# Optimization experiments

Hardware: AMD Instinct MI355X
Metric: run time of the kernel (lower is better)

Reference implementation:

```python
import jax, jax.numpy as jnp
import numpy as np

C = jnp.complex64

def _ry_mat(t):
    c = jnp.cos(t / 2).astype(C)
    s = jnp.sin(t / 2).astype(C)
    return jnp.stack([jnp.stack([c, -s], -1), jnp.stack([s, c], -1)], -2)

def _rx_mat(t):
    c = jnp.cos(t / 2).astype(C)
    s = (-1j) * jnp.sin(t / 2).astype(C)
    return jnp.stack([jnp.stack([c, s], -1), jnp.stack([s, c], -1)], -2)

def _rz_mat(t):
    em = jnp.exp(-1j * (t / 2).astype(C))
    ep = jnp.exp(1j * (t / 2).astype(C))
    z = jnp.zeros_like(em)
    return jnp.stack([jnp.stack([em, z], -1), jnp.stack([z, ep], -1)], -2)

def _apply_1q(psi, gate, w):
    # psi: [bsz, 2^n]; gate: [2,2] (shared) or [bsz,2,2] (per-sample)
    bsz = psi.shape[0]
    s = psi.reshape(bsz, 1 << w, 2, -1)  # wire w isolated on axis 2
    if gate.ndim == 2:
        out = jnp.einsum('ij,bljr->blir', gate, s)
    else:
        out = jnp.einsum('bij,bljr->blir', gate, s)
    return out.reshape(bsz, -1)

def _apply_cnot(psi, c, t):
    bsz = psi.shape[0]
    a, b = min(c, t), max(c, t)
    s = psi.reshape(bsz, 1 << a, 2, 1 << (b - a - 1), 2, -1)
    if c < t:
        # control on axis 2, target on axis 4; after slicing ctrl=1, target -> axis 3
        s = s.at[:, :, 1].set(jnp.flip(s[:, :, 1], axis=3))
    else:
        # control on axis 4, target on axis 2
        s = s.at[:, :, :, :, 1].set(jnp.flip(s[:, :, :, :, 1], axis=2))
    return s.reshape(bsz, -1)

def setup_inputs() -> dict:
    key = jax.random.key(0)
    k1, k2 = jax.random.split(key)
    bsz, n_wires, n_qlayers = 1024, 14, 4
    x_raw = jax.random.normal(k1, (bsz, n_wires), dtype=jnp.float32)
    angles = jax.random.normal(k2, (n_qlayers, n_wires, 3), dtype=jnp.float32) * 0.1
    return {"x_raw": x_raw, "angles": angles}

def reference(x_raw, angles):
    L, n, _ = angles.shape
    bsz = x_raw.shape[0]
    x_enc = jnp.tanh(x_raw[:, :n]) * jnp.pi  # [bsz, n]
    # |0...0> statevector, wire 0 is the most significant bit
    psi = jnp.zeros((bsz, 1 << n), dtype=C).at[:, 0].set(1.0)
    # RY encoding (per-sample angles)
    for w in range(n):
        psi = _apply_1q(psi, _ry_mat(x_enc[:, w]), w)
    # variational layers
    for k in range(L):
        for w in range(n):
            psi = _apply_1q(psi, _rx_mat(angles[k, w, 0]), w)
            psi = _apply_1q(psi, _ry_mat(angles[k, w, 1]), w)
            psi = _apply_1q(psi, _rz_mat(angles[k, w, 2]), w)
        for i in range(n - 1):
            psi = _apply_cnot(psi, i, i + 1)
        psi = _apply_cnot(psi, n - 1, 0)
    # <Z_0>: +|amp|^2 when bit0=0, -|amp|^2 when bit0=1
    p = jnp.abs(psi.reshape(bsz, 2, -1)) ** 2
    return (p[:, 0].sum(-1) - p[:, 1].sum(-1)).astype(jnp.float32)
```

## Files before the change

### kernel.cpp

```cpp
#include <hip/hip_runtime.h>
#include <cmath>
#include <cstdint>

#define NW       14
#define NST      (1 << NW)
#define THREADS  1024
#define NPASS    12
#define WTP      512

typedef _Float16 f16;
typedef _Float16 f16x8 __attribute__((ext_vector_type(8)));
typedef float    f32x4 __attribute__((ext_vector_type(4)));
typedef unsigned short u16;

struct PassArg { u16 Mm[4]; u16 Mt[2]; u16 Mw[4]; };
struct Plan { PassArg ps[NPASS]; u16 initM[14]; u16 measR; u16 _pad; };

__device__ __forceinline__ float2 cmulf(float2 a, float2 b) {
    return make_float2(a.x * b.x - a.y * b.y, a.x * b.y + a.y * b.x);
}
__device__ __host__ __forceinline__ unsigned wtofs(unsigned m, unsigned q01) {
    return (m * 16 + q01 * 8) ^ (((m >> 2) & 1u) << 3);
}

__global__ __launch_bounds__(THREADS, 8)
void vqc_kernel(const float* __restrict__ x_raw, const float* __restrict__ angles,
                float* __restrict__ out, Plan pl)
{
    extern __shared__ char smem[];
    f16*    Sh  = (f16*)smem;
    f16*    Wt  = Sh + 2 * NST;
    float2* Gg  = (float2*)(Wt + NPASS * WTP);
    float2* G0c = Gg + 4 * NW * 4;
    float*  red = (float*)(G0c + 2 * NW);

    const int b   = blockIdx.x;
    const int tid = threadIdx.x;
    const int lane = tid & 63, wv = tid >> 6;
    const int q = lane >> 4, m = lane & 15;

    if (tid < 4 * NW) {
        const int k = tid / NW, w = tid % NW;
        const float a  = angles[(k * NW + w) * 3 + 0];
        const float bb = angles[(k * NW + w) * 3 + 1];
        const float c  = angles[(k * NW + w) * 3 + 2];
        float sa, ca, sb, cb, sc, cc;
        sincosf(a * 0.5f, &sa, &ca);
        sincosf(bb * 0.5f, &sb, &cb);
        sincosf(c * 0.5f, &sc, &cc);
        float2 m00 = make_float2(cb * ca,  sb * sa);
        float2 m01 = make_float2(-sb * ca, -cb * sa);
        float2 m10 = make_float2(sb * ca,  -cb * sa);
        float2 m11 = make_float2(cb * ca,  -sb * sa);
        const float2 e0 = make_float2(cc, -sc), e1 = make_float2(cc, sc);
        const float2 u00 = cmulf(e0, m00), u01 = cmulf(e0, m01);
        const float2 u10 = cmulf(e1, m10), u11 = cmulf(e1, m11);
        const int gi = (k * NW + w) * 4;
        Gg[gi + 0] = u00; Gg[gi + 1] = u01; Gg[gi + 2] = u10; Gg[gi + 3] = u11;
        if (k == 0) {
            const float xe = tanhf(x_raw[b * NW + w]) * 3.14159265358979f;
            float se, ce;
            sincosf(xe * 0.5f, &se, &ce);
            G0c[w * 2 + 0] = make_float2(u00.x * ce + u01.x * se, u00.y * ce + u01.y * se);
            G0c[w * 2 + 1] = make_float2(u10.x * ce + u11.x * se, u10.y * ce + u11.y * se);
        }
    }
    __syncthreads();

    if (tid < 768) {
        const int p = tid >> 6, l6 = tid & 63;
        const int ap = l6 & 15, ahalf = (l6 >> 4) & 1, dup = l6 >> 5;
        const int layer = (p >> 2) + 1, g = p & 3;

        float2 p3;
        if (g == 3) {
            p3 = make_float2((((ap >> 3) & 1) == ahalf) ? 1.f : 0.f, 0.f);
        } else {
            const int wire = 13 - (10 - 4 * g + 3);
            p3 = Gg[(layer * NW + wire) * 4 + ((ap >> 3) & 1) * 2 + ahalf];
        }
        float2 e0a, e0b, e1a, e1b, e2a, e2b;
        {
            const int r0 = ap & 1, r1 = (ap >> 1) & 1, r2 = (ap >> 2) & 1;
            if (g == 3) {
                const float2* G13 = Gg + (layer * NW + 13) * 4;
                const float2* G12 = Gg + (layer * NW + 12) * 4;
                e0a = G13[r0 * 2 + 0]; e0b = G13[r0 * 2 + 1];
                e1a = G12[r1 * 2 + 0]; e1b = G12[r1 * 2 + 1];
                e2a = make_float2(r2 == 0 ? 1.f : 0.f, 0.f);
                e2b = make_float2(r2 == 1 ? 1.f : 0.f, 0.f);
            } else {
                const float2* G0 = Gg + (layer * NW + (13 - (10 - 4 * g + 0))) * 4;
                const float2* G1 = Gg + (layer * NW + (13 - (10 - 4 * g + 1))) * 4;
                const float2* G2 = Gg + (layer * NW + (13 - (10 - 4 * g + 2))) * 4;
                e0a = G0[r0 * 2 + 0]; e0b = G0[r0 * 2 + 1];
                e1a = G1[r1 * 2 + 0]; e1b = G1[r1 * 2 + 1];
                e2a = G2[r2 * 2 + 0]; e2b = G2[r2 * 2 + 1];
            }
        }
        f16x8 frag;
        #pragma unroll
        for (int j2 = 0; j2 < 8; ++j2) {
            float2 v = cmulf(p3, (j2 & 4) ? e2b : e2a);
            v = cmulf(v, (j2 & 2) ? e1b : e1a);
            v = cmulf(v, (j2 & 1) ? e0b : e0a);
            frag[j2] = (f16)(dup ? v.y : v.x);
        }
        *(f16x8*)(Wt + p * WTP + dup * 256 + wtofs(ap, ahalf)) = frag;
    }

    {
        float2 common = make_float2(1.f, 0.f);
        #pragma unroll
        for (int bit = 0; bit < 9; ++bit) {
            const int w = 13 - bit;
            const float2 f = ((tid >> bit) & 1) ? G0c[w * 2 + 1] : G0c[w * 2 + 0];
            common = cmulf(common, f);
        }
        common = cmulf(common, (tid & 512) ? G0c[0 * 2 + 1] : G0c[0 * 2 + 0]);
        unsigned p10 = 0;
        #pragma unroll
        for (int bit = 0; bit < 9; ++bit)
            p10 ^= ((tid >> bit) & 1) ? (unsigned)pl.initM[bit] : 0u;
        if (tid & 512) p10 ^= (unsigned)pl.initM[13];
        const unsigned t9 = (unsigned)pl.initM[9];

        const float2 w4a = G0c[4*2+0], w4b = G0c[4*2+1];
        const float2 w3a = G0c[3*2+0], w3b = G0c[3*2+1];
        const float2 w2a = G0c[2*2+0], w2b = G0c[2*2+1];
        const float2 w1a = G0c[1*2+0], w1b = G0c[1*2+1];

        #pragma unroll
        for (int c = 0; c < 2; ++c) {
            const unsigned ac = p10 ^ (c ? t9 : 0u);
            const unsigned r = ac & 7u;
            const unsigned base = ac & ~7u;
            const bool sA = ((r ^ (unsigned)c) & 1u) != 0;
            const bool sB = ((r ^ (r >> 1)) & 1u) != 0;
            const bool sC = (((r >> 1) ^ (r >> 2)) & 1u) != 0;
            const bool sD = ((r >> 2) & 1u) != 0;
            const float2 A_[2] = { sA ? w4b : w4a, sA ? w4a : w4b };
            const float2 B_[2] = { sB ? w3b : w3a, sB ? w3a : w3b };
            const float2 C_[2] = { sC ? w2b : w2a, sC ? w2a : w2b };
            const float2 D_[2] = { sD ? w1b : w1a, sD ? w1a : w1b };
            const float2 U0  = cmulf(common, A_[0]), U1  = cmulf(common, A_[1]);
            const float2 W00 = cmulf(U0, B_[0]),     W01 = cmulf(U0, B_[1]);
            const float2 W10 = cmulf(U1, B_[1]),     W11 = cmulf(U1, B_[0]);
            const float2 V00 = cmulf(C_[0], D_[0]),  V01 = cmulf(C_[1], D_[1]);
            const float2 V10 = cmulf(C_[1], D_[0]),  V11 = cmulf(C_[0], D_[1]);
            union { f16 h[8]; f16x8 v; } hR, hI;
            float2 amp;
            amp = cmulf(W00, V00); hR.h[0] = (f16)amp.x; hI.h[0] = (f16)amp.y;
            amp = cmulf(W10, V00); hR.h[1] = (f16)amp.x; hI.h[1] = (f16)amp.y;
            amp = cmulf(W01, V10); hR.h[2] = (f16)amp.x; hI.h[2] = (f16)amp.y;
            amp = cmulf(W11, V10); hR.h[3] = (f16)amp.x; hI.h[3] = (f16)amp.y;
            amp = cmulf(W00, V01); hR.h[4] = (f16)amp.x; hI.h[4] = (f16)amp.y;
            amp = cmulf(W10, V01); hR.h[5] = (f16)amp.x; hI.h[5] = (f16)amp.y;
            amp = cmulf(W01, V11); hR.h[6] = (f16)amp.x; hI.h[6] = (f16)amp.y;
            amp = cmulf(W11, V11); hR.h[7] = (f16)amp.x; hI.h[7] = (f16)amp.y;
            *(f16x8*)(Sh + base)       = hR.v;
            *(f16x8*)(Sh + NST + base) = hI.v;
        }
    }
    __syncthreads();

    const unsigned plane_off = (unsigned)(q >> 1) << 14;
    const unsigned q01 = (unsigned)(q & 1);
    const f32x4 z4 = {0.f, 0.f, 0.f, 0.f};
    #pragma unroll
    for (int p = 0; p < NPASS; ++p) {
        const PassArg& P = pl.ps[p];
        const unsigned pm = ((m & 1) ? P.Mm[0] : 0) ^ ((m & 2) ? P.Mm[1] : 0)
                          ^ ((m & 4) ? P.Mm[2] : 0) ^ ((m & 8) ? P.Mm[3] : 0);
        const unsigned wb = ((wv & 1) ? P.Mw[0] : 0) ^ ((wv & 2) ? P.Mw[1] : 0)
                          ^ ((wv & 4) ? P.Mw[2] : 0) ^ ((wv & 8) ? P.Mw[3] : 0);
        const unsigned b0 = pm ^ wb;
        const f16x8 tr = *(const f16x8*)(Wt + p * WTP +       wtofs((unsigned)m, q01));
        const f16x8 ti = *(const f16x8*)(Wt + p * WTP + 256 + wtofs((unsigned)m, q01));
        const f16x8 bf1 = (q < 2) ? tr : -ti;
        const f16x8 bf2 = (q < 2) ? ti : tr;
        unsigned sw[4];
        f16x8 av[4];
        #pragma unroll
        for (int tt = 0; tt < 4; ++tt) {
            sw[tt] = b0 ^ ((tt & 1) ? P.Mt[0] : 0)
                        ^ ((tt & 2) ? P.Mt[1] : 0);
            av[tt] = *(const f16x8*)(Sh + plane_off + (sw[tt] ^ (q01 << 3)));
        }
        #pragma unroll
        for (int tt = 0; tt < 4; ++tt) {
            const f32x4 d1 = __builtin_amdgcn_mfma_f32_16x16x32_f16(av[tt], bf1, z4, 0, 0, 0);
            const f32x4 d2 = __builtin_amdgcn_mfma_f32_16x16x32_f16(av[tt], bf2, z4, 0, 0, 0);
            union { f16 h[4]; uint2 u; } c1, c2;
            #pragma unroll
            for (int r = 0; r < 4; ++r) { c1.h[r] = (f16)d1[r]; c2.h[r] = (f16)d2[r]; }
            const unsigned wu = sw[tt] ^ ((unsigned)q << 2);
            *(uint2*)(Sh + wu)       = c1.u;
            *(uint2*)(Sh + NST + wu) = c2.u;
        }
        __syncthreads();
    }

    float acc = 0.f;
    {
        const unsigned base = (unsigned)tid * 16u;
        const int pb = __popc(base & (unsigned)pl.measR) & 1;
        #pragma unroll
        for (int half = 0; half < 2; ++half) {
            const f16x8 rr = *(const f16x8*)(Sh + base + half * 8);
            const f16x8 ii = *(const f16x8*)(Sh + NST + base + half * 8);
            #pragma unroll
            for (int e = 0; e < 8; ++e) {
                const float re = (float)rr[e], im = (float)ii[e];
                const float pw = fmaf(re, re, im * im);
                const int sgn = pb ^ (__popc((unsigned)(half * 8 + e) & (unsigned)pl.measR) & 1);
                acc += sgn ? -pw : pw;
            }
        }
    }
    #pragma unroll
    for (int off = 32; off > 0; off >>= 1) acc += __shfl_down(acc, off);
    if ((tid & 63) == 0) red[wv] = acc;
    __syncthreads();
    if (tid == 0) {
        float s = 0.f;
        #pragma unroll
        for (int i = 0; i < THREADS / 64; ++i) s += red[i];
        out[b] = s;
    }
}

struct GFm { u16 col[14]; };

static unsigned ringp_host(unsigned x) {
    unsigned s = x;
    s ^= s >> 1; s ^= s >> 2; s ^= s >> 4; s ^= s >> 8;
    s &= 0x3FFFu;
    return (s ^ ((s & 1u) << 13)) & 0x3FFFu;
}
static u16 gf_apply(const GFm& m, u16 v) {
    u16 r = 0;
    for (int b = 0; b < 14; ++b) if ((v >> b) & 1) r ^= m.col[b];
    return r;
}
static GFm gf_compose(const GFm& A, const GFm& B) {
    GFm C;
    for (int b = 0; b < 14; ++b) C.col[b] = gf_apply(A, B.col[b]);
    return C;
}
static void rows_from(const GFm& A, u16 r[14]) {
    for (int i = 0; i < 14; ++i) {
        u16 mm = 0;
        for (int b = 0; b < 14; ++b) mm |= (u16)(((A.col[b] >> i) & 1) << b);
        r[i] = mm;
    }
}
static GFm from_rows(const u16 r[14]) {
    GFm A;
    for (int b = 0; b < 14; ++b) {
        u16 c = 0;
        for (int i = 0; i < 14; ++i) c |= (u16)(((r[i] >> b) & 1) << i);
        A.col[b] = c;
    }
    return A;
}
static GFm gf_inv(const GFm& A) {
    u16 M[14], I[14];
    rows_from(A, M);
    for (int i = 0; i < 14; ++i) I[i] = (u16)(1u << i);
    for (int c = 0; c < 14; ++c) {
        int p = c;
        while (p < 14 && !((M[p] >> c) & 1)) ++p;
        if (p == 14) continue;
        u16 t = M[c]; M[c] = M[p]; M[p] = t;
        t = I[c]; I[c] = I[p]; I[p] = t;
        for (int r2 = 0; r2 < 14; ++r2)
            if (r2 != c && ((M[r2] >> c) & 1)) { M[r2] ^= M[c]; I[r2] ^= I[c]; }
    }
    return from_rows(I);
}

static void build_plan(Plan& pl) {
    GFm ring, ringInv;
    for (int b = 0; b < 14; ++b) ring.col[b] = (u16)ringp_host(1u << b);
    ringInv = gf_inv(ring);

    GFm phi;
    for (int j = 0; j < 4; ++j) phi.col[10 + j] = (u16)(1u << j);
    for (int j = 0; j < 4; ++j) phi.col[6 + j]  = (u16)(1u << (4 + j));
    for (int j = 0; j < 4; ++j) phi.col[2 + j]  = (u16)(1u << (8 + j));
    phi.col[0] = (u16)(1u << 12);
    phi.col[1] = (u16)(1u << 13);

    for (int b = 0; b < 14; ++b) pl.initM[b] = gf_apply(phi, ring.col[b]);

    const int gb[4][4] = {{10,11,12,13},{6,7,8,9},{2,3,4,5},{0,1,6,7}};

    for (int p = 0; p < NPASS; ++p) {
        const int g = p & 3;
        u16 uv[4];
        if (g < 3) for (int j = 0; j < 4; ++j) uv[j] = (u16)(1u << gb[g + 1][j]);
        else       for (int j = 0; j < 4; ++j) uv[j] = ringInv.col[10 + j];
        for (int j = 0; j < 4; ++j) pl.ps[p].Mm[j] = gf_apply(phi, uv[j]);

        u16 span[14]; int ns = 0;
        u16 tv[6]; int nt = 0;
        auto tryAdd = [&](u16 v) -> bool {
            bool ch = true;
            while (ch) {
                ch = false;
                for (int i = 0; i < ns; ++i) {
                    const int tb = 31 - __builtin_clz((unsigned)span[i]);
                    if ((v >> tb) & 1) { v ^= span[i]; ch = true; }
                }
            }
            if (!v) return false;
            span[ns++] = v;
            return true;
        };
        for (int j = 0; j < 4; ++j) tryAdd((u16)(1u << gb[g][j]));
        for (int j = 0; j < 4; ++j) tryAdd(uv[j]);
        for (int b2 = 0; b2 < 14 && nt < 6; ++b2)
            if (tryAdd((u16)(1u << b2))) tv[nt++] = (u16)(1u << b2);
        for (int i = 0; i < 2; ++i) pl.ps[p].Mt[i] = gf_apply(phi, tv[i]);
        for (int i = 0; i < 4; ++i) pl.ps[p].Mw[i] = gf_apply(phi, tv[i + 2]);

        GFm Bm;
        for (int j = 0; j < 4; ++j) Bm.col[j]     = (u16)(1u << gb[g][j]);
        for (int j = 0; j < 4; ++j) Bm.col[4 + j] = uv[j];
        for (int i = 0; i < 6; ++i) Bm.col[8 + i] = tv[i];
        GFm Binv = gf_inv(Bm);
        u16 img[14];
        for (int j = 0; j < 4; ++j) img[j]     = pl.ps[p].Mm[j];
        for (int j = 0; j < 4; ++j) img[4 + j] = (u16)(1u << j);
        for (int i = 0; i < 6; ++i) img[8 + i] = gf_apply(phi, tv[i]);
        GFm nphi;
        for (int b2 = 0; b2 < 14; ++b2) {
            const u16 coef = gf_apply(Binv, (u16)(1u << b2));
            u16 v = 0;
            for (int j = 0; j < 14; ++j) if ((coef >> j) & 1) v ^= img[j];
            nphi.col[b2] = v;
        }
        if (g == 3) nphi = gf_compose(nphi, ringInv);
        phi = nphi;
    }

    GFm pinv = gf_inv(phi);
    u16 rows[14];
    rows_from(pinv, rows);
    pl.measR = rows[13];
    pl._pad = 0;
}

struct SwzP { unsigned c4, c5; unsigned char Lc[8]; };

static unsigned proj35(const SwzP& s, u16 v) {
    unsigned a = ((unsigned)v >> 3) & 7u;
    unsigned r = (a & 1u) ? 1u : 0u;
    if (a & 2u) r ^= s.c4;
    if (a & 4u) r ^= s.c5;
    unsigned hb = ((unsigned)v >> 6) & 0xFFu;
    for (int c = 0; c < 8; ++c) if ((hb >> c) & 1u) r ^= s.Lc[c];
    return r & 7u;
}
static int rank3(const unsigned* q, int n) {
    unsigned bas[3] = {0, 0, 0};
    int r = 0;
    for (int j = 0; j < n; ++j) {
        unsigned v = q[j];
        for (int bit = 2; bit >= 0; --bit) {
            if (!((v >> bit) & 1u)) continue;
            if (bas[bit]) { v ^= bas[bit]; continue; }
            bas[bit] = v; ++r; v = 0; break;
        }
    }
    return r;
}
static bool minv_ok(unsigned c4, unsigned c5) {
    const unsigned q[3] = {1u, c4 & 7u, c5 & 7u};
    return rank3(q, 3) == 3;
}
static int score_swz(const SwzP& s, const u16 MmRaw[NPASS][4]) {
    int bad = 0;
    for (int p = 0; p < NPASS; ++p) {
        unsigned q[4];
        for (int j = 0; j < 4; ++j) q[j] = proj35(s, MmRaw[p][j]);
        bad += 3 - rank3(q, 4);
    }
    return bad;
}
static GFm A_from(const SwzP& s) {
    GFm A;
    for (int b = 0; b < 14; ++b) A.col[b] = (u16)(1u << b);
    A.col[4] = (u16)((s.c4 & 7u) << 3);
    A.col[5] = (u16)((s.c5 & 7u) << 3);
    for (int c = 0; c < 8; ++c)
        A.col[6 + c] = (u16)((1u << (6 + c)) ^ (((unsigned)s.Lc[c] & 7u) << 3));
    return A;
}
static void choose_swz(const Plan& raw, GFm& A, GFm& Ainv) {
    u16 MmRaw[NPASS][4];
    for (int p = 0; p < NPASS; ++p)
        for (int j = 0; j < 4; ++j) MmRaw[p][j] = raw.ps[p].Mm[j];

    SwzP best = {2u, 4u, {1, 2, 4, 1, 2, 5, 2, 4}};
    int bestScore = score_swz(best, MmRaw);

    uint64_t rng = 0x9E3779B97F4A7C15ull;
    auto rnd = [&]() -> unsigned {
        rng = rng * 6364136223846793005ull + 1442695040888963407ull;
        return (unsigned)(rng >> 33);
    };
    for (int t = 0; t < 8000 && bestScore > 0; ++t) {
        SwzP s;
        s.c4 = rnd() & 7u; s.c5 = rnd() & 7u;
        if (!minv_ok(s.c4, s.c5)) continue;
        for (int c = 0; c < 8; ++c) s.Lc[c] = (unsigned char)(rnd() & 7u);
        const int sc = score_swz(s, MmRaw);
        if (sc < bestScore) { bestScore = sc; best = s; }
    }
    A = A_from(best);
    Ainv = gf_inv(A);
}
static void fold_A(Plan& pl, const GFm& A, const GFm& Ainv) {
    for (int p = 0; p < NPASS; ++p) {
        for (int j = 0; j < 4; ++j) pl.ps[p].Mm[j] = gf_apply(A, pl.ps[p].Mm[j]);
        for (int j = 0; j < 2; ++j) pl.ps[p].Mt[j] = gf_apply(A, pl.ps[p].Mt[j]);
        for (int j = 0; j < 4; ++j) pl.ps[p].Mw[j] = gf_apply(A, pl.ps[p].Mw[j]);
    }
    for (int b = 0; b < 14; ++b) pl.initM[b] = gf_apply(A, pl.initM[b]);
    const unsigned r = pl.measR;
    u16 nr = 0;
    for (int b = 0; b < 14; ++b)
        if (__builtin_popcount(r & (unsigned)Ainv.col[b]) & 1) nr |= (u16)(1u << b);
    pl.measR = nr;
}

extern "C" void kernel_launch(void* const* d_in, const int* in_sizes, int n_in,
                              void* d_out, int out_size, void* d_ws, size_t ws_size,
                              hipStream_t stream) {
    const float* x_raw  = (const float*)d_in[0];
    const float* angles = (const float*)d_in[1];
    float* out = (float*)d_out;
    const int bsz = in_sizes[0] / NW;

    Plan pl;
    build_plan(pl);
    GFm A, Ainv;
    choose_swz(pl, A, Ainv);
    fold_A(pl, A, Ainv);

    const size_t lds = (size_t)2 * NST * sizeof(f16)
                     + (size_t)NPASS * WTP * sizeof(f16)
                     + (size_t)(4 * NW * 4) * sizeof(float2)
                     + (size_t)(2 * NW) * sizeof(float2)
                     + (size_t)(THREADS / 64) * sizeof(float);
    (void)hipFuncSetAttribute((const void*)vqc_kernel,
                              hipFuncAttributeMaxDynamicSharedMemorySize, (int)lds);
    vqc_kernel<<<dim3(bsz), dim3(THREADS), lds, stream>>>(x_raw, angles, out, pl);
}
```

Baseline: 118.3 us.

## Precompute shared gate tiles in a prologue kernel and tighten the main pass loop

Adds a single-block pre-kernel that builds the shared fp16 gate fragments and the first-layer unitaries once into workspace memory, so each batch block no longer recomputes them in LDS. The main kernel now reads gate tiles from global memory (cache-resident) and keeps only per-sample encoding work. It also converts MFMA outputs with packed round-toward-zero converts and writes both planes with a single ds_write2st64 instruction, and reorders the final measurement reads for contiguous access. Trade-offs are an extra kernel launch, global loads inside the pass loop, and slightly different fp16 rounding.

```diff
diff --git a/kernel.cpp b/kernel.cpp
--- a/kernel.cpp
+++ b/kernel.cpp
@@ -5,10 +5,12 @@
 #define NW       14
 #define NST      (1 << NW)
 #define THREADS  1024
+#define PRETHR   768
 #define NPASS    12
 #define WTP      512
 
 typedef _Float16 f16;
+typedef __fp16   fp16x2 __attribute__((ext_vector_type(2)));
 typedef _Float16 f16x8 __attribute__((ext_vector_type(8)));
 typedef float    f32x4 __attribute__((ext_vector_type(4)));
 typedef unsigned short u16;
@@ -23,21 +25,12 @@
     return (m * 16 + q01 * 8) ^ (((m >> 2) & 1u) << 3);
 }
 
-__global__ __launch_bounds__(THREADS, 8)
-void vqc_kernel(const float* __restrict__ x_raw, const float* __restrict__ angles,
-                float* __restrict__ out, Plan pl)
+__global__ __launch_bounds__(PRETHR)
+void vqc_pre(const float* __restrict__ angles, f16* __restrict__ wt_g,
+             float2* __restrict__ u0_g)
 {
-    extern __shared__ char smem[];
-    f16*    Sh  = (f16*)smem;
-    f16*    Wt  = Sh + 2 * NST;
-    float2* Gg  = (float2*)(Wt + NPASS * WTP);
-    float2* G0c = Gg + 4 * NW * 4;
-    float*  red = (float*)(G0c + 2 * NW);
-
-    const int b   = blockIdx.x;
+    __shared__ float2 G[4 * NW * 4];
     const int tid = threadIdx.x;
-    const int lane = tid & 63, wv = tid >> 6;
-    const int q = lane >> 4, m = lane & 15;
 
     if (tid < 4 * NW) {
         const int k = tid / NW, w = tid % NW;
@@ -56,18 +49,15 @@
         const float2 u00 = cmulf(e0, m00), u01 = cmulf(e0, m01);
         const float2 u10 = cmulf(e1, m10), u11 = cmulf(e1, m11);
         const int gi = (k * NW + w) * 4;
-        Gg[gi + 0] = u00; Gg[gi + 1] = u01; Gg[gi + 2] = u10; Gg[gi + 3] = u11;
+        G[gi + 0] = u00; G[gi + 1] = u01; G[gi + 2] = u10; G[gi + 3] = u11;
         if (k == 0) {
-            const float xe = tanhf(x_raw[b * NW + w]) * 3.14159265358979f;
-            float se, ce;
-            sincosf(xe * 0.5f, &se, &ce);
-            G0c[w * 2 + 0] = make_float2(u00.x * ce + u01.x * se, u00.y * ce + u01.y * se);
-            G0c[w * 2 + 1] = make_float2(u10.x * ce + u11.x * se, u10.y * ce + u11.y * se);
+            u0_g[w * 4 + 0] = u00; u0_g[w * 4 + 1] = u01;
+            u0_g[w * 4 + 2] = u10; u0_g[w * 4 + 3] = u11;
         }
     }
     __syncthreads();
 
-    if (tid < 768) {
+    {
         const int p = tid >> 6, l6 = tid & 63;
         const int ap = l6 & 15, ahalf = (l6 >> 4) & 1, dup = l6 >> 5;
         const int layer = (p >> 2) + 1, g = p & 3;
@@ -77,22 +67,22 @@
             p3 = make_float2((((ap >> 3) & 1) == ahalf) ? 1.f : 0.f, 0.f);
         } else {
             const int wire = 13 - (10 - 4 * g + 3);
-            p3 = Gg[(layer * NW + wire) * 4 + ((ap >> 3) & 1) * 2 + ahalf];
+            p3 = G[(layer * NW + wire) * 4 + ((ap >> 3) & 1) * 2 + ahalf];
         }
         float2 e0a, e0b, e1a, e1b, e2a, e2b;
         {
             const int r0 = ap & 1, r1 = (ap >> 1) & 1, r2 = (ap >> 2) & 1;
             if (g == 3) {
-                const float2* G13 = Gg + (layer * NW + 13) * 4;
-                const float2* G12 = Gg + (layer * NW + 12) * 4;
+                const float2* G13 = G + (layer * NW + 13) * 4;
+                const float2* G12 = G + (layer * NW + 12) * 4;
                 e0a = G13[r0 * 2 + 0]; e0b = G13[r0 * 2 + 1];
                 e1a = G12[r1 * 2 + 0]; e1b = G12[r1 * 2 + 1];
                 e2a = make_float2(r2 == 0 ? 1.f : 0.f, 0.f);
                 e2b = make_float2(r2 == 1 ? 1.f : 0.f, 0.f);
             } else {
-                const float2* G0 = Gg + (layer * NW + (13 - (10 - 4 * g + 0))) * 4;
-                const float2* G1 = Gg + (layer * NW + (13 - (10 - 4 * g + 1))) * 4;
-                const float2* G2 = Gg + (layer * NW + (13 - (10 - 4 * g + 2))) * 4;
+                const float2* G0 = G + (layer * NW + (13 - (10 - 4 * g + 0))) * 4;
+                const float2* G1 = G + (layer * NW + (13 - (10 - 4 * g + 1))) * 4;
+                const float2* G2 = G + (layer * NW + (13 - (10 - 4 * g + 2))) * 4;
                 e0a = G0[r0 * 2 + 0]; e0b = G0[r0 * 2 + 1];
                 e1a = G1[r1 * 2 + 0]; e1b = G1[r1 * 2 + 1];
                 e2a = G2[r2 * 2 + 0]; e2b = G2[r2 * 2 + 1];
@@ -106,8 +96,34 @@
             v = cmulf(v, (j2 & 1) ? e0b : e0a);
             frag[j2] = (f16)(dup ? v.y : v.x);
         }
-        *(f16x8*)(Wt + p * WTP + dup * 256 + wtofs(ap, ahalf)) = frag;
-    }
+        *(f16x8*)(wt_g + p * WTP + dup * 256 + wtofs(ap, ahalf)) = frag;
+    }
+}
+
+__global__ __launch_bounds__(THREADS, 4)
+void vqc_kernel(const float* __restrict__ x_raw, const f16* __restrict__ wt_g,
+                const float2* __restrict__ u0_g, float* __restrict__ out, Plan pl)
+{
+    extern __shared__ char smem[];
+    f16*    Sh  = (f16*)smem;
+    float2* G0c = (float2*)(Sh + 2 * NST);
+    float*  red = (float*)(G0c + 2 * NW);
+
+    const int b   = blockIdx.x;
+    const int tid = threadIdx.x;
+    const int lane = tid & 63, wv = tid >> 6;
+    const int q = lane >> 4, m = lane & 15;
+
+    if (tid < NW) {
+        const float xe = tanhf(x_raw[b * NW + tid]) * 3.14159265358979f;
+        float se, ce;
+        sincosf(xe * 0.5f, &se, &ce);
+        const float2 u00 = u0_g[tid * 4 + 0], u01 = u0_g[tid * 4 + 1];
+        const float2 u10 = u0_g[tid * 4 + 2], u11 = u0_g[tid * 4 + 3];
+        G0c[tid * 2 + 0] = make_float2(u00.x * ce + u01.x * se, u00.y * ce + u01.y * se);
+        G0c[tid * 2 + 1] = make_float2(u10.x * ce + u11.x * se, u10.y * ce + u11.y * se);
+    }
+    __syncthreads();
 
     {
         float2 common = make_float2(1.f, 0.f);
@@ -166,6 +182,7 @@
 
     const unsigned plane_off = (unsigned)(q >> 1) << 14;
     const unsigned q01 = (unsigned)(q & 1);
+    const f16* wbase = wt_g + wtofs((unsigned)m, q01);
     const f32x4 z4 = {0.f, 0.f, 0.f, 0.f};
     #pragma unroll
     for (int p = 0; p < NPASS; ++p) {
@@ -175,8 +192,8 @@
         const unsigned wb = ((wv & 1) ? P.Mw[0] : 0) ^ ((wv & 2) ? P.Mw[1] : 0)
                           ^ ((wv & 4) ? P.Mw[2] : 0) ^ ((wv & 8) ? P.Mw[3] : 0);
         const unsigned b0 = pm ^ wb;
-        const f16x8 tr = *(const f16x8*)(Wt + p * WTP +       wtofs((unsigned)m, q01));
-        const f16x8 ti = *(const f16x8*)(Wt + p * WTP + 256 + wtofs((unsigned)m, q01));
+        const f16x8 tr = *(const f16x8*)(wbase + p * WTP);
+        const f16x8 ti = *(const f16x8*)(wbase + p * WTP + 256);
         const f16x8 bf1 = (q < 2) ? tr : -ti;
         const f16x8 bf2 = (q < 2) ? ti : tr;
         unsigned sw[4];
@@ -191,29 +208,32 @@
         for (int tt = 0; tt < 4; ++tt) {
             const f32x4 d1 = __builtin_amdgcn_mfma_f32_16x16x32_f16(av[tt], bf1, z4, 0, 0, 0);
             const f32x4 d2 = __builtin_amdgcn_mfma_f32_16x16x32_f16(av[tt], bf2, z4, 0, 0, 0);
-            union { f16 h[4]; uint2 u; } c1, c2;
-            #pragma unroll
-            for (int r = 0; r < 4; ++r) { c1.h[r] = (f16)d1[r]; c2.h[r] = (f16)d2[r]; }
+            union { fp16x2 h2[2]; unsigned long long u; } c1, c2;
+            c1.h2[0] = __builtin_amdgcn_cvt_pkrtz(d1[0], d1[1]);
+            c1.h2[1] = __builtin_amdgcn_cvt_pkrtz(d1[2], d1[3]);
+            c2.h2[0] = __builtin_amdgcn_cvt_pkrtz(d2[0], d2[1]);
+            c2.h2[1] = __builtin_amdgcn_cvt_pkrtz(d2[2], d2[3]);
             const unsigned wu = sw[tt] ^ ((unsigned)q << 2);
-            *(uint2*)(Sh + wu)       = c1.u;
-            *(uint2*)(Sh + NST + wu) = c2.u;
+            const unsigned lds_addr = (unsigned)(uintptr_t)(Sh + wu);
+            asm volatile("ds_write2st64_b64 %0, %1, %2 offset0:0 offset1:64"
+                         :: "v"(lds_addr), "v"(c1.u), "v"(c2.u) : "memory");
         }
         __syncthreads();
     }
 
     float acc = 0.f;
     {
-        const unsigned base = (unsigned)tid * 16u;
-        const int pb = __popc(base & (unsigned)pl.measR) & 1;
-        #pragma unroll
-        for (int half = 0; half < 2; ++half) {
-            const f16x8 rr = *(const f16x8*)(Sh + base + half * 8);
-            const f16x8 ii = *(const f16x8*)(Sh + NST + base + half * 8);
+        #pragma unroll
+        for (int cch = 0; cch < 2; ++cch) {
+            const unsigned addr = (unsigned)cch * 8192u + (unsigned)tid * 8u;
+            const f16x8 rr = *(const f16x8*)(Sh + addr);
+            const f16x8 ii = *(const f16x8*)(Sh + NST + addr);
+            const int pb = __popc(addr & (unsigned)pl.measR) & 1;
             #pragma unroll
             for (int e = 0; e < 8; ++e) {
                 const float re = (float)rr[e], im = (float)ii[e];
                 const float pw = fmaf(re, re, im * im);
-                const int sgn = pb ^ (__popc((unsigned)(half * 8 + e) & (unsigned)pl.measR) & 1);
+                const int sgn = pb ^ (__popc((unsigned)e & (unsigned)pl.measR) & 1);
                 acc += sgn ? -pw : pw;
             }
         }
@@ -450,12 +470,15 @@
     choose_swz(pl, A, Ainv);
     fold_A(pl, A, Ainv);
 
+    f16*    wt_g = (f16*)d_ws;
+    float2* u0_g = (float2*)((char*)d_ws + (size_t)NPASS * WTP * sizeof(f16));
+
+    vqc_pre<<<dim3(1), dim3(PRETHR), 0, stream>>>(angles, wt_g, u0_g);
+
     const size_t lds = (size_t)2 * NST * sizeof(f16)
-                     + (size_t)NPASS * WTP * sizeof(f16)
-                     + (size_t)(4 * NW * 4) * sizeof(float2)
                      + (size_t)(2 * NW) * sizeof(float2)
                      + (size_t)(THREADS / 64) * sizeof(float);
     (void)hipFuncSetAttribute((const void*)vqc_kernel,
                               hipFuncAttributeMaxDynamicSharedMemorySize, (int)lds);
-    vqc_kernel<<<dim3(bsz), dim3(THREADS), lds, stream>>>(x_raw, angles, out, pl);
-}
+    vqc_kernel<<<dim3(bsz), dim3(THREADS), lds, stream>>>(x_raw, wt_g, u0_g, out, pl);
+}
```

Result: no change. 119.4 us (+0.9%).
